# Kernel tuning notes

Hardware: AMD Instinct MI355X
Metric: run time of the kernel (lower is better)

Reference implementation:

```python
import jax, jax.numpy as jnp
import numpy as np

B, M, D, V = 2048, 64, 256, 50000  # batch, max neighbors, embed dim, num_symbols (pad idx = V)
EPS = 1e-5


def _ln(x, g, b):
    mu = jnp.mean(x, axis=-1, keepdims=True)
    var = jnp.var(x, axis=-1, keepdims=True)
    return (x - mu) * jax.lax.rsqrt(var + EPS) * g + b


def _attn(q, k, v, Wq, Wk, Wv, Wb, Wo, bo):
    # q: (B, D); k, v: (B, M, D). num_heads=1, att_size=D. NOTE: self.scale is defined
    # but never used in the original forward, so no scaling here (faithful).
    qh = q @ Wq.T                                   # (B, D)
    kh = jnp.einsum('bmd,ed->bme', k, Wk)           # (B, M, D)
    vh = jnp.einsum('bmd,ed->bme', v, Wv)           # (B, M, D)
    s = jnp.einsum('bd,bmd->bm', qh @ Wb.T, kh)     # bilinear-modulated scores
    a = jax.nn.softmax(s, axis=-1)
    o = jnp.einsum('bm,bmd->bd', a, vh)
    return o @ Wo.T + bo


def setup_inputs() -> dict:
    key = jax.random.key(0)
    ks = jax.random.split(key, 40)
    f = lambda i, shape, s=0.05: (jax.random.normal(ks[i], shape, dtype=jnp.float32) * s)
    emb = f(0, (V + 1, D), 0.1).at[V].set(0.0)  # padding_idx row is zero
    inp = {
        'entity_pairs': jax.random.randint(ks[1], (B, 2), 0, V),
        'left_conn': jax.random.randint(ks[2], (B, M, 2), 0, V),
        'left_deg': jax.random.randint(ks[3], (B,), 0, M),
        'right_conn': jax.random.randint(ks[4], (B, M, 2), 0, V),
        'right_deg': jax.random.randint(ks[5], (B,), 0, M),
        'emb': emb,
        # task-aware attention params
        'Wq_t': f(6, (D, D)), 'Wk_t': f(7, (D, D)), 'Wv_t': f(8, (D, D)),
        'Wbil_t': f(9, (D, D)), 'Wo_t': f(10, (D, D)), 'bo_t': jnp.zeros((D,), jnp.float32),
        # entity-pair attention params
        'Wq_e': f(11, (D, D)), 'Wk_e': f(12, (D, D)), 'Wv_e': f(13, (D, D)),
        'Wbil_e': f(14, (D, D)), 'Wo_e': f(15, (D, D)), 'bo_e': jnp.zeros((D,), jnp.float32),
        'ln_g': jnp.ones((D,), jnp.float32), 'ln_b': jnp.zeros((D,), jnp.float32),
        'Wtail': f(16, (D, D)), 'Whead': f(17, (D, D)),
        'Wrel': f(18, (2 * D, D, D), 0.02),  # nn.Bilinear weight (out, in1, in2), no bias
        'W1': f(19, (2 * D, 2 * D)), 'b1': jnp.zeros((2 * D,), jnp.float32),
        'W2': f(20, (2 * D, 2 * D)),
        'ln1_g': jnp.ones((2 * D,), jnp.float32), 'ln1_b': jnp.zeros((2 * D,), jnp.float32),
        'Wg': f(21, (D, D), 0.3), 'Ug': f(22, (D, D), 0.3), 'bg': jnp.zeros((D,), jnp.float32),
        'Wr': f(23, (D, D), 0.3), 'Ur': f(24, (D, D), 0.3), 'br': jnp.zeros((D,), jnp.float32),
    }
    return inp


def reference(entity_pairs, left_conn, left_deg, right_conn, right_deg, emb,
              Wq_t, Wk_t, Wv_t, Wbil_t, Wo_t, bo_t,
              Wq_e, Wk_e, Wv_e, Wbil_e, Wo_e, bo_e,
              ln_g, ln_b, Wtail, Whead, Wrel, W1, b1, W2, ln1_g, ln1_b,
              Wg, Ug, bg, Wr, Ur, br):
    # eval mode: dropouts are identity
    ent = emb[entity_pairs]                 # (B, 2, D)
    eL, eR = ent[:, 0], ent[:, 1]           # (B, D) each
    rel_L = emb[left_conn[:, :, 0]]         # (B, M, D)
    ent_L = emb[left_conn[:, :, 1]]
    rel_R = emb[right_conn[:, :, 0]]
    ent_R = emb[right_conn[:, :, 1]]

    # rel_w bilinear: (B, 2D) -> split into forward/backward task relation embeddings
    rel_emb = jnp.einsum('bi,oij,bj->bo', eL, Wrel, eR)
    rel_fwd, rel_bwd = rel_emb[:, :D], rel_emb[:, D:]

    # GRU-style neighbor gating
    g = jax.nn.sigmoid(rel_L @ Wg + ent_L @ Ug + bg)
    V_head = jax.nn.relu(g * rel_L + (1.0 - g) * ent_L)
    gr = jax.nn.sigmoid(rel_R @ Wr + ent_R @ Ur + br)
    V_tail = jax.nn.relu(gr * rel_R + (1.0 - gr) * ent_R)

    def enhance(att_out, e):
        h = jax.nn.relu(att_out @ Wtail.T + e @ Whead.T)
        return _ln(h + e, ln_g, ln_b)

    h_rel = _attn(rel_fwd, rel_L, V_head, Wq_t, Wk_t, Wv_t, Wbil_t, Wo_t, bo_t)
    enh_head_ = enhance(h_rel, eL)
    t_rel = _attn(rel_bwd, rel_R, V_tail, Wq_t, Wk_t, Wv_t, Wbil_t, Wo_t, bo_t)
    enh_tail_ = enhance(t_rel, eR)

    h_ent = _attn(enh_tail_, ent_L, V_head, Wq_e, Wk_e, Wv_e, Wbil_e, Wo_e, bo_e)
    enh_head = enhance(h_ent, eL)
    t_ent = _attn(enh_head_, ent_R, V_tail, Wq_e, Wk_e, Wv_e, Wbil_e, Wo_e, bo_e)
    enh_tail = enhance(t_ent, eR)

    pair = jnp.concatenate([enh_head, enh_tail], axis=-1)  # (B, 2D)
    # bi_MLP with residual + LayerNorm
    h = jax.nn.relu(pair @ W1.T + b1)
    h = h @ W2.T
    return _ln(h + pair, ln1_g, ln1_b)
```

## Files before the change

### kernel.cpp

```cpp
#include <hip/hip_runtime.h>
#include <hip/hip_bf16.h>

#define BN 2048
#define MN 64
#define DN 256
#define EMB_ROWS 50001
#define EMB_PAD 50016
#define LN_EPS 1e-5f
#define SPLITK 16

typedef __hip_bfloat16 bf16;
typedef __attribute__((ext_vector_type(8))) short bf16x8;
typedef __attribute__((ext_vector_type(4))) float f32x4;

static __device__ __forceinline__ short f2bf(float f) {
  return __builtin_bit_cast(short, __float2bfloat16(f));
}
static __device__ __forceinline__ float bfu(unsigned short u) {
  unsigned int x = ((unsigned int)u) << 16;
  return __builtin_bit_cast(float, x);
}

typedef __attribute__((address_space(1))) const void g_void;
typedef __attribute__((address_space(3))) void l_void;
static __device__ __forceinline__ void gl_lds16(const void* g, void* l) {
  __builtin_amdgcn_global_load_lds((g_void*)g, (l_void*)l, 16, 0, 0);
}

static __device__ __forceinline__ void dev_mm(float* __restrict__ C, const float* __restrict__ A,
                                              const float* __restrict__ B, int N, int K,
                                              int aI, int aM, int bM, int bJ, int blk, int tid) {
  int idx = blk * 256 + tid;
  int i = idx / N, j = idx - i * N;
  float s = 0.f;
  for (int m = 0; m < K; ++m) s += A[i * aI + m * aM] * B[m * bM + j * bJ];
  C[idx] = s;
}
static __device__ __forceinline__ void dev_tr(float* __restrict__ dst, const float* __restrict__ src,
                                              int rows, int cols, int blk, int tid) {
  int idx = blk * 256 + tid;
  int r = idx / cols, c = idx - r * cols;
  dst[c * rows + r] = src[idx];
}

#define S1_GRID 27349
__global__ void k_stage1(const float* __restrict__ Wbil_t, const float* __restrict__ Wq_t,
                         const float* __restrict__ Wbil_e, const float* __restrict__ Wq_e,
                         const float* __restrict__ Wo_t, const float* __restrict__ Wv_t,
                         const float* __restrict__ Wo_e, const float* __restrict__ Wv_e,
                         const float* __restrict__ Wtail, const float* __restrict__ Whead,
                         const float* __restrict__ W1, const float* __restrict__ W2,
                         const float* __restrict__ Wg, const float* __restrict__ Ug,
                         const float* __restrict__ Wr, const float* __restrict__ Ur,
                         const float* __restrict__ Wrel, const float* __restrict__ emb,
                         const int* __restrict__ pairs,
                         float* __restrict__ T_t, float* __restrict__ T_e,
                         float* __restrict__ Wov_t, float* __restrict__ Wov_e,
                         float* __restrict__ WtailT, float* __restrict__ Whead_kn,
                         float* __restrict__ W1_kn, float* __restrict__ W2_kn,
                         bf16* __restrict__ wcat, bf16* __restrict__ emb_bf,
                         float* __restrict__ eL, float* __restrict__ eR,
                         bf16* __restrict__ eRbf, float* __restrict__ eLT,
                         bf16* __restrict__ Wrel_bf) {
  int bid = blockIdx.x, tid = threadIdx.x;
  if (bid < 256)        dev_mm(T_t, Wbil_t, Wq_t, 256, 256, 256, 1, 256, 1, bid, tid);
  else if (bid < 512)   dev_mm(T_e, Wbil_e, Wq_e, 256, 256, 256, 1, 256, 1, bid - 256, tid);
  else if (bid < 768)   dev_mm(Wov_t, Wo_t, Wv_t, 256, 256, 256, 1, 256, 1, bid - 512, tid);
  else if (bid < 1024)  dev_mm(Wov_e, Wo_e, Wv_e, 256, 256, 256, 1, 256, 1, bid - 768, tid);
  else if (bid < 1280)  dev_tr(WtailT, Wtail, 256, 256, bid - 1024, tid);
  else if (bid < 1536)  dev_tr(Whead_kn, Whead, 256, 256, bid - 1280, tid);
  else if (bid < 2560)  dev_tr(W1_kn, W1, 512, 512, bid - 1536, tid);
  else if (bid < 3584)  dev_tr(W2_kn, W2, 512, 512, bid - 2560, tid);
  else if (bid < 4608) {
    int idx = (bid - 3584) * 256 + tid;
    int n = idx >> 8, k = idx & 255;
    const float* s = (n < 256) ? Wg : (n < 512) ? Ug : (n < 768) ? Wr : Ur;
    wcat[idx] = __float2bfloat16(s[k * 256 + (n & 255)]);
  } else if (bid < 17109) {
    int i = (bid - 4608) * 256 + tid;
    if (i < (EMB_ROWS * 256) / 4) {
      float4 v = ((const float4*)emb)[i];
      ushort4 o;
      o.x = (unsigned short)f2bf(v.x); o.y = (unsigned short)f2bf(v.y);
      o.z = (unsigned short)f2bf(v.z); o.w = (unsigned short)f2bf(v.w);
      ((ushort4*)emb_bf)[i] = o;
    }
  } else if (bid < 19157) {
    int b = bid - 17109, d = tid;
    float vL = emb[(size_t)pairs[2 * b] * 256 + d];
    float vR = emb[(size_t)pairs[2 * b + 1] * 256 + d];
    eL[b * 256 + d] = vL;
    eR[b * 256 + d] = vR;
    eRbf[b * 256 + d] = __float2bfloat16(vR);
    eLT[(size_t)d * BN + b] = vL;
  } else {
    int blk = bid - 19157;
    int base = blk * 1024 + tid;
    #pragma unroll
    for (int it = 0; it < 4; ++it) {
      int i = base + it * 256;
      float4 v = ((const float4*)Wrel)[i];
      ushort4 o;
      o.x = (unsigned short)f2bf(v.x); o.y = (unsigned short)f2bf(v.y);
      o.z = (unsigned short)f2bf(v.z); o.w = (unsigned short)f2bf(v.w);
      ((ushort4*)Wrel_bf)[i] = o;
    }
  }
}

__global__ void k_stage2(const float* __restrict__ T_t, const float* __restrict__ Wk_t, float* __restrict__ Cq_t,
                         const float* __restrict__ T_e, const float* __restrict__ Wk_e, float* __restrict__ Cq_e,
                         const float* __restrict__ Wov_t, const float* __restrict__ WtailT, float* __restrict__ Wenh_t,
                         const float* __restrict__ Wov_e, float* __restrict__ Wenh_e,
                         const float* __restrict__ Wtail, const float* __restrict__ bo_t, const float* __restrict__ bo_e,
                         float* __restrict__ benh_t, float* __restrict__ benh_e) {
  int bid = blockIdx.x, tid = threadIdx.x;
  if (bid < 256)       dev_mm(Cq_t, T_t, Wk_t, 256, 256, 1, 256, 256, 1, bid, tid);
  else if (bid < 512)  dev_mm(Cq_e, T_e, Wk_e, 256, 256, 1, 256, 256, 1, bid - 256, tid);
  else if (bid < 768)  dev_mm(Wenh_t, Wov_t, WtailT, 256, 256, 1, 256, 256, 1, bid - 512, tid);
  else if (bid < 1024) dev_mm(Wenh_e, Wov_e, WtailT, 256, 256, 1, 256, 256, 1, bid - 768, tid);
  else {
    float s1 = 0.f, s2 = 0.f;
    for (int m = 0; m < 256; ++m) {
      float w = Wtail[tid * 256 + m];
      s1 += w * bo_t[m];
      s2 += w * bo_e[m];
    }
    benh_t[tid] = s1;
    benh_e[tid] = s2;
  }
}

__global__ __launch_bounds__(256, 2) void k_e4_gemm(const bf16* __restrict__ embbf,
                                                    const bf16* __restrict__ wcat,
                                                    bf16* __restrict__ E4) {
  int bid = blockIdx.x;
  int lid = (bid & 7) * 392 + (bid >> 3);
  int mchunk = lid >> 4, nt = lid & 15;
  int tid = threadIdx.x;
  int w = tid >> 6, lane = tid & 63;
  int l16 = lane & 15, lq = lane >> 4, kfo = lq * 8;
  int n0 = nt * 64;

  bf16x8 B[4][8];
  #pragma unroll
  for (int nf = 0; nf < 4; ++nf) {
    const bf16* bp = wcat + (size_t)(n0 + nf * 16 + l16) * 256 + kfo;
    #pragma unroll
    for (int ks = 0; ks < 8; ++ks) B[nf][ks] = *(const bf16x8*)(bp + ks * 32);
  }

  f32x4 z = {0.f, 0.f, 0.f, 0.f};
  #pragma unroll
  for (int g = 0; g < 4; ++g) {
    int rbase = mchunk * 256 + w * 64 + g * 16;
    int arow = rbase + l16; if (arow >= EMB_ROWS) arow = EMB_ROWS - 1;
    const bf16* ap = embbf + (size_t)arow * 256 + kfo;
    bf16x8 A[8];
    #pragma unroll
    for (int ks = 0; ks < 8; ++ks) A[ks] = *(const bf16x8*)(ap + ks * 32);
    f32x4 acc[4];
    #pragma unroll
    for (int nf = 0; nf < 4; ++nf) acc[nf] = z;
    #pragma unroll
    for (int ks = 0; ks < 8; ++ks) {
      acc[0] = __builtin_amdgcn_mfma_f32_16x16x32_bf16(A[ks], B[0][ks], acc[0], 0, 0, 0);
      acc[1] = __builtin_amdgcn_mfma_f32_16x16x32_bf16(A[ks], B[1][ks], acc[1], 0, 0, 0);
      acc[2] = __builtin_amdgcn_mfma_f32_16x16x32_bf16(A[ks], B[2][ks], acc[2], 0, 0, 0);
      acc[3] = __builtin_amdgcn_mfma_f32_16x16x32_bf16(A[ks], B[3][ks], acc[3], 0, 0, 0);
    }
    #pragma unroll
    for (int nf = 0; nf < 4; ++nf) {
      int col = n0 + nf * 16 + l16;
      #pragma unroll
      for (int r = 0; r < 4; ++r) {
        int row = rbase + lq * 4 + r;
        if (row < EMB_ROWS) E4[(size_t)row * 1024 + col] = __float2bfloat16(acc[nf][r]);
      }
    }
  }
}

__global__ __launch_bounds__(256, 2) void k_bilinear(const bf16* __restrict__ eRbf,
                                                     const float* __restrict__ eLT,
                                                     const bf16* __restrict__ wrel,
                                                     float* __restrict__ part) {
  __shared__ char bsh[2][8192];
  int bid = blockIdx.x;
  int lid = (bid & 7) * 256 + (bid >> 3);
  int bx = lid & 15, by = (lid >> 4) & 7, bz = lid >> 7;
  int tid = threadIdx.x, w = tid >> 6, lane = tid & 63;
  int l16 = lane & 15, lq = lane >> 4;
  int kfo = lq * 8;
  int m_base = bx * 128 + w * 32;
  int n0 = by * 64;
  int i0 = bz * 16;

  bf16x8 ar[2][8];
  #pragma unroll
  for (int mi = 0; mi < 2; ++mi) {
    const bf16* er = eRbf + (size_t)(m_base + mi * 16 + l16) * 256 + kfo;
    #pragma unroll
    for (int jb = 0; jb < 8; ++jb) ar[mi][jb] = *(const bf16x8*)(er + jb * 32);
  }

  f32x4 z = {0.f, 0.f, 0.f, 0.f};
  f32x4 accF[2][4];
  f32x4 P[2][4];
  #pragma unroll
  for (int mi = 0; mi < 2; ++mi)
    #pragma unroll
    for (int nf = 0; nf < 4; ++nf) { accF[mi][nf] = z; P[mi][nf] = z; }

  int srow = tid >> 3, sblk = tid & 7;
  const bf16* wbase = wrel + (size_t)n0 * 65536 + (size_t)i0 * 256;
  auto stage = [&](int c, int step) {
    size_t so = (size_t)step * 64;
    #pragma unroll
    for (int q = 0; q < 2; ++q) {
      int r = q * 32 + srow;
      const bf16* src = wbase + (size_t)r * 65536 + so + (size_t)((sblk ^ (r & 7)) << 3);
      gl_lds16(src, &bsh[c][q * 4096 + w * 1024]);
    }
  };

  stage(0, 0);
  __syncthreads();
  int cur = 0;
  for (int s = 0; s < 16; ++s) {
    const float* elb = eLT + (size_t)(i0 + s) * BN + m_base + lq * 4;
    float4 el0 = *(const float4*)(elb);
    float4 el1 = *(const float4*)(elb + 16);
    #pragma unroll
    for (int jb4 = 0; jb4 < 4; ++jb4) {
      int step = s * 4 + jb4;
      if (step + 1 < 64) stage(cur ^ 1, step + 1);
      bf16x8 bq[2][4];
      #pragma unroll
      for (int kk = 0; kk < 2; ++kk)
        #pragma unroll
        for (int nf = 0; nf < 4; ++nf) {
          int rl = nf * 16 + l16;
          int blk = (kk * 4 + lq) ^ (l16 & 7);
          bq[kk][nf] = *(const bf16x8*)&bsh[cur][rl * 128 + (blk << 4)];
        }
      #pragma unroll
      for (int kk = 0; kk < 2; ++kk)
        #pragma unroll
        for (int mi = 0; mi < 2; ++mi)
          #pragma unroll
          for (int nf = 0; nf < 4; ++nf) {
            if (jb4 == 0 && kk == 0)
              P[mi][nf] = __builtin_amdgcn_mfma_f32_16x16x32_bf16(ar[mi][jb4 * 2 + kk], bq[kk][nf], z, 0, 0, 0);
            else
              P[mi][nf] = __builtin_amdgcn_mfma_f32_16x16x32_bf16(ar[mi][jb4 * 2 + kk], bq[kk][nf], P[mi][nf], 0, 0, 0);
          }
      __syncthreads();
      cur ^= 1;
    }
    #pragma unroll
    for (int mi = 0; mi < 2; ++mi) {
      float4 el = mi ? el1 : el0;
      #pragma unroll
      for (int nf = 0; nf < 4; ++nf) {
        accF[mi][nf][0] += el.x * P[mi][nf][0];
        accF[mi][nf][1] += el.y * P[mi][nf][1];
        accF[mi][nf][2] += el.z * P[mi][nf][2];
        accF[mi][nf][3] += el.w * P[mi][nf][3];
      }
    }
  }

  float* p = part + (size_t)bz * BN * 512;
  #pragma unroll
  for (int mi = 0; mi < 2; ++mi) {
    #pragma unroll
    for (int nf = 0; nf < 4; ++nf) {
      int col = n0 + nf * 16 + l16;
      #pragma unroll
      for (int r = 0; r < 4; ++r) {
        int row = m_base + mi * 16 + lq * 4 + r;
        p[(size_t)row * 512 + col] = accF[mi][nf][r];
      }
    }
  }
}

__global__ __launch_bounds__(256) void k_vbuild(const int* __restrict__ lconn, const int* __restrict__ rconn,
                                                const bf16* __restrict__ embbf, const bf16* __restrict__ E4,
                                                const float* __restrict__ bg, const float* __restrict__ br,
                                                bf16* __restrict__ Vh, bf16* __restrict__ Vt) {
  int task = blockIdx.x * 4 + (threadIdx.x >> 6);
  int lane = threadIdx.x & 63;
  int d0 = lane * 4;
  {
    int i0 = lconn[2 * task], i1 = lconn[2 * task + 1];
    ushort4 ga = *(const ushort4*)(E4 + (size_t)i0 * 1024 + d0);
    ushort4 gb = *(const ushort4*)(E4 + (size_t)i1 * 1024 + 256 + d0);
    float4 bgv = *(const float4*)(bg + d0);
    ushort4 ea = *(const ushort4*)(embbf + (size_t)i0 * 256 + d0);
    ushort4 eb = *(const ushort4*)(embbf + (size_t)i1 * 256 + d0);
    ushort4 oh;
    {
      float g = 1.f / (1.f + expf(-(bfu(ga.x) + bfu(gb.x) + bgv.x)));
      oh.x = (unsigned short)f2bf(fmaxf(g * bfu(ea.x) + (1.f - g) * bfu(eb.x), 0.f));
      g = 1.f / (1.f + expf(-(bfu(ga.y) + bfu(gb.y) + bgv.y)));
      oh.y = (unsigned short)f2bf(fmaxf(g * bfu(ea.y) + (1.f - g) * bfu(eb.y), 0.f));
      g = 1.f / (1.f + expf(-(bfu(ga.z) + bfu(gb.z) + bgv.z)));
      oh.z = (unsigned short)f2bf(fmaxf(g * bfu(ea.z) + (1.f - g) * bfu(eb.z), 0.f));
      g = 1.f / (1.f + expf(-(bfu(ga.w) + bfu(gb.w) + bgv.w)));
      oh.w = (unsigned short)f2bf(fmaxf(g * bfu(ea.w) + (1.f - g) * bfu(eb.w), 0.f));
    }
    *(ushort4*)(Vh + (size_t)task * 256 + d0) = oh;
  }
  {
    int r0 = rconn[2 * task], r1 = rconn[2 * task + 1];
    ushort4 ga = *(const ushort4*)(E4 + (size_t)r0 * 1024 + 512 + d0);
    ushort4 gb = *(const ushort4*)(E4 + (size_t)r1 * 1024 + 768 + d0);
    float4 brv = *(const float4*)(br + d0);
    ushort4 ea = *(const ushort4*)(embbf + (size_t)r0 * 256 + d0);
    ushort4 eb = *(const ushort4*)(embbf + (size_t)r1 * 256 + d0);
    ushort4 ot;
    {
      float g = 1.f / (1.f + expf(-(bfu(ga.x) + bfu(gb.x) + brv.x)));
      ot.x = (unsigned short)f2bf(fmaxf(g * bfu(ea.x) + (1.f - g) * bfu(eb.x), 0.f));
      g = 1.f / (1.f + expf(-(bfu(ga.y) + bfu(gb.y) + brv.y)));
      ot.y = (unsigned short)f2bf(fmaxf(g * bfu(ea.y) + (1.f - g) * bfu(eb.y), 0.f));
      g = 1.f / (1.f + expf(-(bfu(ga.z) + bfu(gb.z) + brv.z)));
      ot.z = (unsigned short)f2bf(fmaxf(g * bfu(ea.z) + (1.f - g) * bfu(eb.z), 0.f));
      g = 1.f / (1.f + expf(-(bfu(ga.w) + bfu(gb.w) + brv.w)));
      ot.w = (unsigned short)f2bf(fmaxf(g * bfu(ea.w) + (1.f - g) * bfu(eb.w), 0.f));
    }
    *(ushort4*)(Vt + (size_t)task * 256 + d0) = ot;
  }
}

__global__ __launch_bounds__(256) void k_qk12(const float* __restrict__ part, const float* __restrict__ Cq,
                                              float* __restrict__ qkb) {
  __shared__ float xs[16][256];
  int bid = blockIdx.x, tid = threadIdx.x;
  int half = bid >> 7;
  int r0 = (bid & 127) * 16;
  int col0 = half * 256;
  for (int t = tid; t < 16 * 256; t += 256) {
    int r = t >> 8, k = t & 255;
    const float* pp = part + (size_t)(r0 + r) * 512 + col0 + k;
    float s = 0.f;
    #pragma unroll
    for (int z = 0; z < SPLITK; ++z) s += pp[(size_t)z * BN * 512];
    xs[r][k] = s;
  }
  __syncthreads();
  float acc[16];
  #pragma unroll
  for (int r = 0; r < 16; ++r) acc[r] = 0.f;
  for (int k4 = 0; k4 < 256; k4 += 4) {
    float w0 = Cq[(k4 + 0) * 256 + tid];
    float w1 = Cq[(k4 + 1) * 256 + tid];
    float w2 = Cq[(k4 + 2) * 256 + tid];
    float w3 = Cq[(k4 + 3) * 256 + tid];
    #pragma unroll
    for (int r = 0; r < 16; ++r) {
      float4 a = *(const float4*)&xs[r][k4];
      acc[r] += a.x * w0 + a.y * w1 + a.z * w2 + a.w * w3;
    }
  }
  int ob = half * 2048 + r0;
  #pragma unroll
  for (int r = 0; r < 16; ++r) qkb[(size_t)(ob + r) * 256 + tid] = acc[r];
}

__global__ __launch_bounds__(256) void k_qk34(const float* __restrict__ X0, const float* __restrict__ X1,
                                              const float* __restrict__ Cq, float* __restrict__ qkb) {
  __shared__ float xs[16][256];
  int bid = blockIdx.x, tid = threadIdx.x;
  int half = bid >> 7;
  const float* X = half ? X1 : X0;
  int r0 = (bid & 127) * 16;
  for (int t = tid; t < 16 * 256; t += 256) {
    int r = t >> 8, k = t & 255;
    xs[r][k] = X[(size_t)(r0 + r) * 256 + k];
  }
  __syncthreads();
  float acc[16];
  #pragma unroll
  for (int r = 0; r < 16; ++r) acc[r] = 0.f;
  for (int k4 = 0; k4 < 256; k4 += 4) {
    float w0 = Cq[(k4 + 0) * 256 + tid];
    float w1 = Cq[(k4 + 1) * 256 + tid];
    float w2 = Cq[(k4 + 2) * 256 + tid];
    float w3 = Cq[(k4 + 3) * 256 + tid];
    #pragma unroll
    for (int r = 0; r < 16; ++r) {
      float4 a = *(const float4*)&xs[r][k4];
      acc[r] += a.x * w0 + a.y * w1 + a.z * w2 + a.w * w3;
    }
  }
  int ob = half * 2048 + r0;
  #pragma unroll
  for (int r = 0; r < 16; ++r) qkb[(size_t)(ob + r) * 256 + tid] = acc[r];
}

__global__ __launch_bounds__(256) void k_attn_dual(const float* __restrict__ qk,
                                                   const int* __restrict__ lconn, const int* __restrict__ rconn,
                                                   const bf16* __restrict__ Vh, const bf16* __restrict__ Vt,
                                                   int sel, const bf16* __restrict__ embbf,
                                                   float* __restrict__ ov) {
  __shared__ float ss[64];
  __shared__ float as[64];
  __shared__ float ps[4][256];
  int bid = blockIdx.x;
  int b = bid & 2047;
  const int* conn = (bid < 2048) ? lconn : rconn;
  const bf16* Vbuf = (bid < 2048) ? Vh : Vt;
  int tid = threadIdx.x;
  int w = tid >> 6, lane = tid & 63;
  float4 qv = *(const float4*)(qk + (size_t)bid * 256 + lane * 4);
  for (int mi = 0; mi < 16; ++mi) {
    int m = w * 16 + mi;
    int idx = conn[((size_t)b * 64 + m) * 2 + sel];
    ushort4 kr = *(const ushort4*)(embbf + (size_t)idx * 256 + lane * 4);
    float p = qv.x * bfu(kr.x) + qv.y * bfu(kr.y) + qv.z * bfu(kr.z) + qv.w * bfu(kr.w);
    #pragma unroll
    for (int off = 32; off; off >>= 1) p += __shfl_xor(p, off, 64);
    if (lane == 0) ss[m] = p;
  }
  __syncthreads();
  if (w == 0) {
    float v = ss[lane];
    float mx = v;
    #pragma unroll
    for (int off = 32; off; off >>= 1) mx = fmaxf(mx, __shfl_xor(mx, off, 64));
    float e = expf(v - mx);
    float sum = e;
    #pragma unroll
    for (int off = 32; off; off >>= 1) sum += __shfl_xor(sum, off, 64);
    as[lane] = e / sum;
  }
  __syncthreads();
  const bf16* vrow = Vbuf + (size_t)b * 64 * 256;
  float4 a4 = {0.f, 0.f, 0.f, 0.f};
  for (int mi = 0; mi < 16; ++mi) {
    int m = w * 16 + mi;
    float sc = as[m];
    ushort4 v4 = *(const ushort4*)(vrow + (size_t)m * 256 + lane * 4);
    a4.x += sc * bfu(v4.x);
    a4.y += sc * bfu(v4.y);
    a4.z += sc * bfu(v4.z);
    a4.w += sc * bfu(v4.w);
  }
  *(float4*)&ps[w][lane * 4] = a4;
  __syncthreads();
  float o = ps[0][tid] + ps[1][tid] + ps[2][tid] + ps[3][tid];
  ov[(size_t)bid * 256 + tid] = o;
}

__global__ __launch_bounds__(256) void k_enh_dual(const float* __restrict__ ovb,
                                                  const float* __restrict__ e0, const float* __restrict__ e1,
                                                  const float* __restrict__ Wenh_kn, const float* __restrict__ Whead_kn,
                                                  const float* __restrict__ benh, const float* __restrict__ lng,
                                                  const float* __restrict__ lnb,
                                                  float* __restrict__ out0, float* __restrict__ out1,
                                                  int ostride, int ob0, int ob1) {
  __shared__ float x1[16][256];
  __shared__ float x2[16][256];
  __shared__ float stats[16][2];
  int bid = blockIdx.x, tid = threadIdx.x;
  int half = bid >> 7;
  const float* e = half ? e1 : e0;
  float* outp = half ? out1 : out0;
  int obase = half ? ob1 : ob0;
  int r0 = (bid & 127) * 16;
  int ovr0 = half * 2048 + r0;
  for (int t = tid; t < 16 * 256; t += 256) {
    int r = t >> 8, k = t & 255;
    x1[r][k] = ovb[(size_t)(ovr0 + r) * 256 + k];
    x2[r][k] = e[(size_t)(r0 + r) * 256 + k];
  }
  __syncthreads();
  float acc[16];
  #pragma unroll
  for (int r = 0; r < 16; ++r) acc[r] = 0.f;
  for (int k4 = 0; k4 < 256; k4 += 4) {
    float w10 = Wenh_kn[(k4 + 0) * 256 + tid], w11 = Wenh_kn[(k4 + 1) * 256 + tid];
    float w12 = Wenh_kn[(k4 + 2) * 256 + tid], w13 = Wenh_kn[(k4 + 3) * 256 + tid];
    float w20 = Whead_kn[(k4 + 0) * 256 + tid], w21 = Whead_kn[(k4 + 1) * 256 + tid];
    float w22 = Whead_kn[(k4 + 2) * 256 + tid], w23 = Whead_kn[(k4 + 3) * 256 + tid];
    #pragma unroll
    for (int r = 0; r < 16; ++r) {
      float4 a = *(const float4*)&x1[r][k4];
      float4 bb = *(const float4*)&x2[r][k4];
      acc[r] += a.x * w10 + a.y * w11 + a.z * w12 + a.w * w13
              + bb.x * w20 + bb.y * w21 + bb.z * w22 + bb.w * w23;
    }
  }
  float bz = benh[tid];
  float hv[16];
  #pragma unroll
  for (int r = 0; r < 16; ++r) hv[r] = fmaxf(acc[r] + bz, 0.f) + x2[r][tid];
  __syncthreads();
  #pragma unroll
  for (int r = 0; r < 16; ++r) x1[r][tid] = hv[r];
  __syncthreads();
  int w = tid >> 6, lane = tid & 63;
  for (int rr = 0; rr < 4; ++rr) {
    int r = w * 4 + rr;
    float s1 = 0.f, s2 = 0.f;
    #pragma unroll
    for (int jj = 0; jj < 4; ++jj) {
      float v = x1[r][lane + jj * 64];
      s1 += v; s2 += v * v;
    }
    #pragma unroll
    for (int off = 32; off; off >>= 1) {
      s1 += __shfl_xor(s1, off, 64);
      s2 += __shfl_xor(s2, off, 64);
    }
    if (lane == 0) {
      float mu = s1 * (1.f / 256.f);
      float var = s2 * (1.f / 256.f) - mu * mu;
      stats[r][0] = mu;
      stats[r][1] = rsqrtf(var + LN_EPS);
    }
  }
  __syncthreads();
  float gv = lng[tid], bv = lnb[tid];
  #pragma unroll
  for (int r = 0; r < 16; ++r) {
    float v = (x1[r][tid] - stats[r][0]) * stats[r][1] * gv + bv;
    outp[(size_t)(r0 + r) * ostride + obase + tid] = v;
  }
}

__global__ __launch_bounds__(256) void k_lin(const float* __restrict__ X, const float* __restrict__ Wkn,
                                             const float* __restrict__ bias, float* __restrict__ Y,
                                             int Kdim, int Ndim, int act) {
  __shared__ float xs[16][512];
  int tid = threadIdx.x;
  int r0 = blockIdx.x * 16;
  int col = blockIdx.y * 256 + tid;
  for (int t = tid; t < 16 * Kdim; t += 256) {
    int r = t / Kdim, k = t - r * Kdim;
    xs[r][k] = X[(size_t)(r0 + r) * Kdim + k];
  }
  __syncthreads();
  float acc[16];
  #pragma unroll
  for (int r = 0; r < 16; ++r) acc[r] = 0.f;
  for (int k4 = 0; k4 < Kdim; k4 += 4) {
    float w0 = Wkn[(size_t)(k4 + 0) * Ndim + col];
    float w1 = Wkn[(size_t)(k4 + 1) * Ndim + col];
    float w2 = Wkn[(size_t)(k4 + 2) * Ndim + col];
    float w3 = Wkn[(size_t)(k4 + 3) * Ndim + col];
    #pragma unroll
    for (int r = 0; r < 16; ++r) {
      float4 a = *(const float4*)&xs[r][k4];
      acc[r] += a.x * w0 + a.y * w1 + a.z * w2 + a.w * w3;
    }
  }
  float bv = bias ? bias[col] : 0.f;
  #pragma unroll
  for (int r = 0; r < 16; ++r) {
    float v = acc[r] + bv;
    if (act) v = fmaxf(v, 0.f);
    Y[(size_t)(r0 + r) * Ndim + col] = v;
  }
}

__global__ __launch_bounds__(256) void k_mlp2ln(const float* __restrict__ h1, const float* __restrict__ W2kn,
                                                const float* __restrict__ pairb, const float* __restrict__ g,
                                                const float* __restrict__ bb, float* __restrict__ out) {
  __shared__ float xs[16][512];
  __shared__ float stats[16][2];
  int bid = blockIdx.x, tid = threadIdx.x;
  int r0 = bid * 16;
  for (int t = tid; t < 16 * 512; t += 256) {
    int r = t >> 9, k = t & 511;
    xs[r][k] = h1[(size_t)(r0 + r) * 512 + k];
  }
  __syncthreads();
  float acc0[16], acc1[16];
  #pragma unroll
  for (int r = 0; r < 16; ++r) { acc0[r] = 0.f; acc1[r] = 0.f; }
  for (int k4 = 0; k4 < 512; k4 += 4) {
    float a0 = W2kn[(size_t)(k4 + 0) * 512 + tid];
    float a1 = W2kn[(size_t)(k4 + 1) * 512 + tid];
    float a2 = W2kn[(size_t)(k4 + 2) * 512 + tid];
    float a3 = W2kn[(size_t)(k4 + 3) * 512 + tid];
    float b0 = W2kn[(size_t)(k4 + 0) * 512 + tid + 256];
    float b1 = W2kn[(size_t)(k4 + 1) * 512 + tid + 256];
    float b2 = W2kn[(size_t)(k4 + 2) * 512 + tid + 256];
    float b3 = W2kn[(size_t)(k4 + 3) * 512 + tid + 256];
    #pragma unroll
    for (int r = 0; r < 16; ++r) {
      float4 a = *(const float4*)&xs[r][k4];
      acc0[r] += a.x * a0 + a.y * a1 + a.z * a2 + a.w * a3;
      acc1[r] += a.x * b0 + a.y * b1 + a.z * b2 + a.w * b3;
    }
  }
  __syncthreads();
  #pragma unroll
  for (int r = 0; r < 16; ++r) {
    xs[r][tid]       = acc0[r] + pairb[(size_t)(r0 + r) * 512 + tid];
    xs[r][tid + 256] = acc1[r] + pairb[(size_t)(r0 + r) * 512 + tid + 256];
  }
  __syncthreads();
  int w = tid >> 6, lane = tid & 63;
  for (int rr = 0; rr < 4; ++rr) {
    int r = w * 4 + rr;
    float s1 = 0.f, s2 = 0.f;
    #pragma unroll
    for (int jj = 0; jj < 8; ++jj) {
      float v = xs[r][lane + jj * 64];
      s1 += v; s2 += v * v;
    }
    #pragma unroll
    for (int off = 32; off; off >>= 1) {
      s1 += __shfl_xor(s1, off, 64);
      s2 += __shfl_xor(s2, off, 64);
    }
    if (lane == 0) {
      float mu = s1 * (1.f / 512.f);
      stats[r][0] = mu;
      stats[r][1] = rsqrtf(s2 * (1.f / 512.f) - mu * mu + LN_EPS);
    }
  }
  __syncthreads();
  float g0 = g[tid], g1 = g[tid + 256], b0v = bb[tid], b1v = bb[tid + 256];
  #pragma unroll
  for (int r = 0; r < 16; ++r) {
    float mu = stats[r][0], rstd = stats[r][1];
    out[(size_t)(r0 + r) * 512 + tid]       = (xs[r][tid] - mu) * rstd * g0 + b0v;
    out[(size_t)(r0 + r) * 512 + tid + 256] = (xs[r][tid + 256] - mu) * rstd * g1 + b1v;
  }
}

extern "C" void kernel_launch(void* const* d_in, const int* in_sizes, int n_in,
                              void* d_out, int out_size, void* d_ws, size_t ws_size,
                              hipStream_t stream) {
  (void)in_sizes; (void)n_in; (void)out_size; (void)ws_size;
  const int*   entity_pairs = (const int*)d_in[0];
  const int*   left_conn    = (const int*)d_in[1];
  const int*   right_conn   = (const int*)d_in[3];
  const float* emb    = (const float*)d_in[5];
  const float* Wq_t   = (const float*)d_in[6];
  const float* Wk_t   = (const float*)d_in[7];
  const float* Wv_t   = (const float*)d_in[8];
  const float* Wbil_t = (const float*)d_in[9];
  const float* Wo_t   = (const float*)d_in[10];
  const float* bo_t   = (const float*)d_in[11];
  const float* Wq_e   = (const float*)d_in[12];
  const float* Wk_e   = (const float*)d_in[13];
  const float* Wv_e   = (const float*)d_in[14];
  const float* Wbil_e = (const float*)d_in[15];
  const float* Wo_e   = (const float*)d_in[16];
  const float* bo_e   = (const float*)d_in[17];
  const float* ln_g   = (const float*)d_in[18];
  const float* ln_b   = (const float*)d_in[19];
  const float* Wtail  = (const float*)d_in[20];
  const float* Whead  = (const float*)d_in[21];
  const float* Wrel   = (const float*)d_in[22];
  const float* W1     = (const float*)d_in[23];
  const float* b1     = (const float*)d_in[24];
  const float* W2     = (const float*)d_in[25];
  const float* ln1_g  = (const float*)d_in[26];
  const float* ln1_b  = (const float*)d_in[27];
  const float* Wg     = (const float*)d_in[28];
  const float* Ug     = (const float*)d_in[29];
  const float* bg     = (const float*)d_in[30];
  const float* Wr     = (const float*)d_in[31];
  const float* Ur     = (const float*)d_in[32];
  const float* br     = (const float*)d_in[33];
  float* out = (float*)d_out;

  char* wp = (char*)d_ws;
  auto alloc = [&](size_t bytes) -> void* {
    void* p = (void*)wp;
    wp += (bytes + 255) & ~(size_t)255;
    return p;
  };
  bf16* Wrel_bf = (bf16*)alloc((size_t)512 * 65536 * 2);
  bf16* emb_bf  = (bf16*)alloc((size_t)EMB_PAD * 256 * 2);
  bf16* E4      = (bf16*)alloc((size_t)EMB_PAD * 1024 * 2);
  bf16* wcat    = (bf16*)alloc((size_t)1024 * 256 * 2);
  bf16* Vh      = (bf16*)alloc((size_t)BN * MN * 256 * 2);
  bf16* Vt      = (bf16*)alloc((size_t)BN * MN * 256 * 2);
  bf16* eRbf_g  = (bf16*)alloc((size_t)BN * 256 * 2);
  float* eLT    = (float*)alloc((size_t)256 * BN * 4);
  float* eLp     = (float*)alloc((size_t)BN * 256 * 4);
  float* eRp     = (float*)alloc((size_t)BN * 256 * 4);
  float* bil_part= (float*)alloc((size_t)SPLITK * BN * 512 * 4);
  float* qkbuf   = (float*)alloc((size_t)2 * BN * 256 * 4);
  float* ovbuf   = (float*)alloc((size_t)2 * BN * 256 * 4);
  float* enh_h   = (float*)alloc((size_t)BN * 256 * 4);
  float* enh_t   = (float*)alloc((size_t)BN * 256 * 4);
  float* pairb   = (float*)alloc((size_t)BN * 512 * 4);
  float* h1buf   = (float*)alloc((size_t)BN * 512 * 4);
  float* T_t     = (float*)alloc(256 * 256 * 4);
  float* Cq_t    = (float*)alloc(256 * 256 * 4);
  float* Wov_t   = (float*)alloc(256 * 256 * 4);
  float* Wenh_t  = (float*)alloc(256 * 256 * 4);
  float* benh_t  = (float*)alloc(256 * 4);
  float* T_e     = (float*)alloc(256 * 256 * 4);
  float* Cq_e    = (float*)alloc(256 * 256 * 4);
  float* Wov_e   = (float*)alloc(256 * 256 * 4);
  float* Wenh_e  = (float*)alloc(256 * 256 * 4);
  float* benh_e  = (float*)alloc(256 * 4);
  float* Whead_kn= (float*)alloc(256 * 256 * 4);
  float* WtailT  = (float*)alloc(256 * 256 * 4);
  float* W1_kn   = (float*)alloc(512 * 512 * 4);
  float* W2_kn   = (float*)alloc(512 * 512 * 4);

  k_stage1<<<S1_GRID, 256, 0, stream>>>(Wbil_t, Wq_t, Wbil_e, Wq_e, Wo_t, Wv_t, Wo_e, Wv_e,
                                        Wtail, Whead, W1, W2, Wg, Ug, Wr, Ur, Wrel, emb,
                                        entity_pairs,
                                        T_t, T_e, Wov_t, Wov_e, WtailT, Whead_kn, W1_kn, W2_kn,
                                        wcat, emb_bf, eLp, eRp, eRbf_g, eLT, Wrel_bf);
  k_stage2<<<1025, 256, 0, stream>>>(T_t, Wk_t, Cq_t, T_e, Wk_e, Cq_e,
                                     Wov_t, WtailT, Wenh_t, Wov_e, Wenh_e,
                                     Wtail, bo_t, bo_e, benh_t, benh_e);
  k_e4_gemm<<<3136, 256, 0, stream>>>(emb_bf, wcat, E4);
  k_bilinear<<<2048, 256, 0, stream>>>(eRbf_g, eLT, Wrel_bf, bil_part);
  k_vbuild<<<(BN * MN) / 4, 256, 0, stream>>>(left_conn, right_conn, emb_bf, E4, bg, br, Vh, Vt);

  k_qk12<<<256, 256, 0, stream>>>(bil_part, Cq_t, qkbuf);
  k_attn_dual<<<4096, 256, 0, stream>>>(qkbuf, left_conn, right_conn, Vh, Vt, 0, emb_bf, ovbuf);
  k_enh_dual<<<256, 256, 0, stream>>>(ovbuf, eLp, eRp, Wenh_t, Whead_kn, benh_t, ln_g, ln_b,
                                      enh_h, enh_t, 256, 0, 0);
  k_qk34<<<256, 256, 0, stream>>>(enh_t, enh_h, Cq_e, qkbuf);
  k_attn_dual<<<4096, 256, 0, stream>>>(qkbuf, left_conn, right_conn, Vh, Vt, 1, emb_bf, ovbuf);
  k_enh_dual<<<256, 256, 0, stream>>>(ovbuf, eLp, eRp, Wenh_e, Whead_kn, benh_e, ln_g, ln_b,
                                      pairb, pairb, 512, 0, 256);

  k_lin<<<dim3(128, 2), 256, 0, stream>>>(pairb, W1_kn, b1, h1buf, 512, 512, 1);
  k_mlp2ln<<<128, 256, 0, stream>>>(h1buf, W2_kn, pairb, ln1_g, ln1_b, out);
}
```

Before: 980.6 us.

## Merge stage2, E4 GEMM and bilinear into one launch with deeper LDS pipeline

Combines the weight-precompute kernel, the embedding projection GEMM and the bilinear relation kernel into a single heterogeneous launch, so that independent work can run at the same time and fewer launch boundaries are paid. The vbuild and qk12 kernels are also merged into one launch. The bilinear kernel now processes 32 input rows per block, halving split-K from 16 to 8 and shrinking the partial-sum buffer. It uses a 4-deep global-to-LDS ring buffer with explicit vmcnt waits and raw barriers instead of double buffering. The cost is more LDS per block (32KB), which may limit occupancy for the co-scheduled E4 and dev_mm blocks, and fewer bilinear blocks for parallelism.

```diff
diff --git a/kernel.cpp b/kernel.cpp
--- a/kernel.cpp
+++ b/kernel.cpp
@@ -7,7 +7,9 @@
 #define EMB_ROWS 50001
 #define EMB_PAD 50016
 #define LN_EPS 1e-5f
-#define SPLITK 16
+#define SPLITK 8
+#define KCHUNK 8192
+#define TSTEPS 128
 
 typedef __hip_bfloat16 bf16;
 typedef __attribute__((ext_vector_type(8))) short bf16x8;
@@ -108,33 +110,120 @@
   }
 }
 
-__global__ void k_stage2(const float* __restrict__ T_t, const float* __restrict__ Wk_t, float* __restrict__ Cq_t,
-                         const float* __restrict__ T_e, const float* __restrict__ Wk_e, float* __restrict__ Cq_e,
-                         const float* __restrict__ Wov_t, const float* __restrict__ WtailT, float* __restrict__ Wenh_t,
-                         const float* __restrict__ Wov_e, float* __restrict__ Wenh_e,
-                         const float* __restrict__ Wtail, const float* __restrict__ bo_t, const float* __restrict__ bo_e,
-                         float* __restrict__ benh_t, float* __restrict__ benh_e) {
-  int bid = blockIdx.x, tid = threadIdx.x;
-  if (bid < 256)       dev_mm(Cq_t, T_t, Wk_t, 256, 256, 1, 256, 256, 1, bid, tid);
-  else if (bid < 512)  dev_mm(Cq_e, T_e, Wk_e, 256, 256, 1, 256, 256, 1, bid - 256, tid);
-  else if (bid < 768)  dev_mm(Wenh_t, Wov_t, WtailT, 256, 256, 1, 256, 256, 1, bid - 512, tid);
-  else if (bid < 1024) dev_mm(Wenh_e, Wov_e, WtailT, 256, 256, 1, 256, 256, 1, bid - 768, tid);
-  else {
-    float s1 = 0.f, s2 = 0.f;
-    for (int m = 0; m < 256; ++m) {
-      float w = Wtail[tid * 256 + m];
-      s1 += w * bo_t[m];
-      s2 += w * bo_e[m];
-    }
-    benh_t[tid] = s1;
-    benh_e[tid] = s2;
-  }
-}
-
-__global__ __launch_bounds__(256, 2) void k_e4_gemm(const bf16* __restrict__ embbf,
-                                                    const bf16* __restrict__ wcat,
-                                                    bf16* __restrict__ E4) {
-  int bid = blockIdx.x;
+static __device__ __forceinline__ void dev_bilinear(char (*bsh)[8192], int bid,
+                                                    const bf16* __restrict__ eRbf,
+                                                    const float* __restrict__ eLT,
+                                                    const bf16* __restrict__ wrel,
+                                                    float* __restrict__ part) {
+  int lid = (bid & 7) * 128 + (bid >> 3);
+  int bx = lid & 15, by = (lid >> 4) & 7, bz = lid >> 7;
+  int tid = threadIdx.x, w = tid >> 6, lane = tid & 63;
+  int l16 = lane & 15, lq = lane >> 4;
+  int kfo = lq * 8;
+  int m_base = bx * 128 + w * 32;
+  int n0 = by * 64;
+  int i0 = bz * 32;
+
+  bf16x8 ar[2][8];
+  #pragma unroll
+  for (int mi = 0; mi < 2; ++mi) {
+    const bf16* er = eRbf + (size_t)(m_base + mi * 16 + l16) * 256 + kfo;
+    #pragma unroll
+    for (int jb = 0; jb < 8; ++jb) ar[mi][jb] = *(const bf16x8*)(er + jb * 32);
+  }
+
+  f32x4 z = {0.f, 0.f, 0.f, 0.f};
+  f32x4 accF[2][4];
+  f32x4 P[2][4];
+  #pragma unroll
+  for (int mi = 0; mi < 2; ++mi)
+    #pragma unroll
+    for (int nf = 0; nf < 4; ++nf) { accF[mi][nf] = z; P[mi][nf] = z; }
+
+  int srow = tid >> 3, sblk = tid & 7;
+  const bf16* wbase = wrel + (size_t)n0 * 65536 + (size_t)i0 * 256;
+  auto stage = [&](int c, int step) {
+    size_t so = (size_t)step * 64;
+    #pragma unroll
+    for (int q = 0; q < 2; ++q) {
+      int r = q * 32 + srow;
+      const bf16* src = wbase + (size_t)r * 65536 + so + (size_t)((sblk ^ (r & 7)) << 3);
+      gl_lds16(src, &bsh[c][q * 4096 + w * 1024]);
+    }
+  };
+
+  stage(0, 0); stage(1, 1); stage(2, 2);
+  float4 el0 = {0,0,0,0}, el1 = {0,0,0,0};
+  for (int t = 0; t < TSTEPS; ++t) {
+    if ((t & 3) == 0) {
+      int s = t >> 2;
+      const float* elb = eLT + (size_t)(i0 + s) * BN + m_base + lq * 4;
+      el0 = *(const float4*)(elb);
+      el1 = *(const float4*)(elb + 16);
+      #pragma unroll
+      for (int mi = 0; mi < 2; ++mi)
+        #pragma unroll
+        for (int nf = 0; nf < 4; ++nf) P[mi][nf] = z;
+    }
+    if (t + 3 < TSTEPS) stage((t + 3) & 3, t + 3);
+    __builtin_amdgcn_sched_barrier(0);
+    if (t + 3 < TSTEPS) { asm volatile("s_waitcnt vmcnt(6)" ::: "memory"); }
+    else                { asm volatile("s_waitcnt vmcnt(0)" ::: "memory"); }
+    __builtin_amdgcn_s_barrier();
+    __builtin_amdgcn_sched_barrier(0);
+    const char* bufp = bsh[t & 3];
+    #pragma unroll
+    for (int kk = 0; kk < 2; ++kk) {
+      bf16x8 bq[4];
+      #pragma unroll
+      for (int nf = 0; nf < 4; ++nf) {
+        int rl = nf * 16 + l16;
+        int blk = (kk * 4 + lq) ^ (l16 & 7);
+        bq[nf] = *(const bf16x8*)&bufp[rl * 128 + (blk << 4)];
+      }
+      int jb = (t & 3) * 2 + kk;
+      #pragma unroll
+      for (int mi = 0; mi < 2; ++mi)
+        #pragma unroll
+        for (int nf = 0; nf < 4; ++nf)
+          P[mi][nf] = __builtin_amdgcn_mfma_f32_16x16x32_bf16(ar[mi][jb], bq[nf], P[mi][nf], 0, 0, 0);
+    }
+    if ((t & 3) == 3) {
+      #pragma unroll
+      for (int mi = 0; mi < 2; ++mi) {
+        float4 el = mi ? el1 : el0;
+        #pragma unroll
+        for (int nf = 0; nf < 4; ++nf) {
+          accF[mi][nf][0] += el.x * P[mi][nf][0];
+          accF[mi][nf][1] += el.y * P[mi][nf][1];
+          accF[mi][nf][2] += el.z * P[mi][nf][2];
+          accF[mi][nf][3] += el.w * P[mi][nf][3];
+        }
+      }
+    }
+    __builtin_amdgcn_sched_barrier(0);
+    asm volatile("s_waitcnt lgkmcnt(0)" ::: "memory");
+    __builtin_amdgcn_s_barrier();
+    __builtin_amdgcn_sched_barrier(0);
+  }
+
+  float* p = part + (size_t)bz * BN * 512;
+  #pragma unroll
+  for (int mi = 0; mi < 2; ++mi) {
+    #pragma unroll
+    for (int nf = 0; nf < 4; ++nf) {
+      int col = n0 + nf * 16 + l16;
+      #pragma unroll
+      for (int r = 0; r < 4; ++r) {
+        int row = m_base + mi * 16 + lq * 4 + r;
+        p[(size_t)row * 512 + col] = accF[mi][nf][r];
+      }
+    }
+  }
+}
+
+static __device__ __forceinline__ void dev_e4(int bid, const bf16* __restrict__ embbf,
+                                              const bf16* __restrict__ wcat, bf16* __restrict__ E4) {
   int lid = (bid & 7) * 392 + (bid >> 3);
   int mchunk = lid >> 4, nt = lid & 15;
   int tid = threadIdx.x;
@@ -181,116 +270,51 @@
   }
 }
 
-__global__ __launch_bounds__(256, 2) void k_bilinear(const bf16* __restrict__ eRbf,
-                                                     const float* __restrict__ eLT,
-                                                     const bf16* __restrict__ wrel,
-                                                     float* __restrict__ part) {
-  __shared__ char bsh[2][8192];
-  int bid = blockIdx.x;
-  int lid = (bid & 7) * 256 + (bid >> 3);
-  int bx = lid & 15, by = (lid >> 4) & 7, bz = lid >> 7;
-  int tid = threadIdx.x, w = tid >> 6, lane = tid & 63;
-  int l16 = lane & 15, lq = lane >> 4;
-  int kfo = lq * 8;
-  int m_base = bx * 128 + w * 32;
-  int n0 = by * 64;
-  int i0 = bz * 16;
-
-  bf16x8 ar[2][8];
-  #pragma unroll
-  for (int mi = 0; mi < 2; ++mi) {
-    const bf16* er = eRbf + (size_t)(m_base + mi * 16 + l16) * 256 + kfo;
-    #pragma unroll
-    for (int jb = 0; jb < 8; ++jb) ar[mi][jb] = *(const bf16x8*)(er + jb * 32);
-  }
-
-  f32x4 z = {0.f, 0.f, 0.f, 0.f};
-  f32x4 accF[2][4];
-  f32x4 P[2][4];
-  #pragma unroll
-  for (int mi = 0; mi < 2; ++mi)
-    #pragma unroll
-    for (int nf = 0; nf < 4; ++nf) { accF[mi][nf] = z; P[mi][nf] = z; }
-
-  int srow = tid >> 3, sblk = tid & 7;
-  const bf16* wbase = wrel + (size_t)n0 * 65536 + (size_t)i0 * 256;
-  auto stage = [&](int c, int step) {
-    size_t so = (size_t)step * 64;
-    #pragma unroll
-    for (int q = 0; q < 2; ++q) {
-      int r = q * 32 + srow;
-      const bf16* src = wbase + (size_t)r * 65536 + so + (size_t)((sblk ^ (r & 7)) << 3);
-      gl_lds16(src, &bsh[c][q * 4096 + w * 1024]);
-    }
-  };
-
-  stage(0, 0);
-  __syncthreads();
-  int cur = 0;
-  for (int s = 0; s < 16; ++s) {
-    const float* elb = eLT + (size_t)(i0 + s) * BN + m_base + lq * 4;
-    float4 el0 = *(const float4*)(elb);
-    float4 el1 = *(const float4*)(elb + 16);
-    #pragma unroll
-    for (int jb4 = 0; jb4 < 4; ++jb4) {
-      int step = s * 4 + jb4;
-      if (step + 1 < 64) stage(cur ^ 1, step + 1);
-      bf16x8 bq[2][4];
-      #pragma unroll
-      for (int kk = 0; kk < 2; ++kk)
-        #pragma unroll
-        for (int nf = 0; nf < 4; ++nf) {
-          int rl = nf * 16 + l16;
-          int blk = (kk * 4 + lq) ^ (l16 & 7);
-          bq[kk][nf] = *(const bf16x8*)&bsh[cur][rl * 128 + (blk << 4)];
-        }
-      #pragma unroll
-      for (int kk = 0; kk < 2; ++kk)
-        #pragma unroll
-        for (int mi = 0; mi < 2; ++mi)
-          #pragma unroll
-          for (int nf = 0; nf < 4; ++nf) {
-            if (jb4 == 0 && kk == 0)
-              P[mi][nf] = __builtin_amdgcn_mfma_f32_16x16x32_bf16(ar[mi][jb4 * 2 + kk], bq[kk][nf], z, 0, 0, 0);
-            else
-              P[mi][nf] = __builtin_amdgcn_mfma_f32_16x16x32_bf16(ar[mi][jb4 * 2 + kk], bq[kk][nf], P[mi][nf], 0, 0, 0);
-          }
-      __syncthreads();
-      cur ^= 1;
-    }
-    #pragma unroll
-    for (int mi = 0; mi < 2; ++mi) {
-      float4 el = mi ? el1 : el0;
-      #pragma unroll
-      for (int nf = 0; nf < 4; ++nf) {
-        accF[mi][nf][0] += el.x * P[mi][nf][0];
-        accF[mi][nf][1] += el.y * P[mi][nf][1];
-        accF[mi][nf][2] += el.z * P[mi][nf][2];
-        accF[mi][nf][3] += el.w * P[mi][nf][3];
+__global__ __launch_bounds__(256, 2) void k_heavy(const bf16* __restrict__ eRbf, const float* __restrict__ eLT,
+                                                  const bf16* __restrict__ wrel, float* __restrict__ part,
+                                                  const bf16* __restrict__ embbf, const bf16* __restrict__ wcat,
+                                                  bf16* __restrict__ E4,
+                                                  const float* __restrict__ T_t, const float* __restrict__ Wk_t,
+                                                  float* __restrict__ Cq_t,
+                                                  const float* __restrict__ T_e, const float* __restrict__ Wk_e,
+                                                  float* __restrict__ Cq_e,
+                                                  const float* __restrict__ Wov_t, const float* __restrict__ WtailT,
+                                                  float* __restrict__ Wenh_t,
+                                                  const float* __restrict__ Wov_e, float* __restrict__ Wenh_e,
+                                                  const float* __restrict__ Wtail, const float* __restrict__ bo_t,
+                                                  const float* __restrict__ bo_e,
+                                                  float* __restrict__ benh_t, float* __restrict__ benh_e) {
+  __shared__ char bsh[4][8192];
+  int bid = blockIdx.x, tid = threadIdx.x;
+  if (bid < 1024) {
+    dev_bilinear(bsh, bid, eRbf, eLT, wrel, part);
+  } else if (bid < 4160) {
+    dev_e4(bid - 1024, embbf, wcat, E4);
+  } else {
+    int b2 = bid - 4160;
+    if (b2 < 256)       dev_mm(Cq_t, T_t, Wk_t, 256, 256, 1, 256, 256, 1, b2, tid);
+    else if (b2 < 512)  dev_mm(Cq_e, T_e, Wk_e, 256, 256, 1, 256, 256, 1, b2 - 256, tid);
+    else if (b2 < 768)  dev_mm(Wenh_t, Wov_t, WtailT, 256, 256, 1, 256, 256, 1, b2 - 512, tid);
+    else if (b2 < 1024) dev_mm(Wenh_e, Wov_e, WtailT, 256, 256, 1, 256, 256, 1, b2 - 768, tid);
+    else {
+      float s1 = 0.f, s2 = 0.f;
+      for (int m = 0; m < 256; ++m) {
+        float wv = Wtail[tid * 256 + m];
+        s1 += wv * bo_t[m];
+        s2 += wv * bo_e[m];
       }
-    }
-  }
-
-  float* p = part + (size_t)bz * BN * 512;
-  #pragma unroll
-  for (int mi = 0; mi < 2; ++mi) {
-    #pragma unroll
-    for (int nf = 0; nf < 4; ++nf) {
-      int col = n0 + nf * 16 + l16;
-      #pragma unroll
-      for (int r = 0; r < 4; ++r) {
-        int row = m_base + mi * 16 + lq * 4 + r;
-        p[(size_t)row * 512 + col] = accF[mi][nf][r];
-      }
-    }
-  }
-}
-
-__global__ __launch_bounds__(256) void k_vbuild(const int* __restrict__ lconn, const int* __restrict__ rconn,
-                                                const bf16* __restrict__ embbf, const bf16* __restrict__ E4,
-                                                const float* __restrict__ bg, const float* __restrict__ br,
-                                                bf16* __restrict__ Vh, bf16* __restrict__ Vt) {
-  int task = blockIdx.x * 4 + (threadIdx.x >> 6);
+      benh_t[tid] = s1;
+      benh_e[tid] = s2;
+    }
+  }
+}
+
+static __device__ __forceinline__ void dev_vbuild(int bid, const int* __restrict__ lconn,
+                                                  const int* __restrict__ rconn,
+                                                  const bf16* __restrict__ embbf, const bf16* __restrict__ E4,
+                                                  const float* __restrict__ bg, const float* __restrict__ br,
+                                                  bf16* __restrict__ Vh, bf16* __restrict__ Vt) {
+  int task = bid * 4 + (threadIdx.x >> 6);
   int lane = threadIdx.x & 63;
   int d0 = lane * 4;
   {
@@ -335,19 +359,28 @@
   }
 }
 
-__global__ __launch_bounds__(256) void k_qk12(const float* __restrict__ part, const float* __restrict__ Cq,
-                                              float* __restrict__ qkb) {
+__global__ __launch_bounds__(256) void k_vq(const int* __restrict__ lconn, const int* __restrict__ rconn,
+                                            const bf16* __restrict__ embbf, const bf16* __restrict__ E4,
+                                            const float* __restrict__ bg, const float* __restrict__ br,
+                                            bf16* __restrict__ Vh, bf16* __restrict__ Vt,
+                                            const float* __restrict__ part, const float* __restrict__ Cq,
+                                            float* __restrict__ qkb) {
   __shared__ float xs[16][256];
   int bid = blockIdx.x, tid = threadIdx.x;
-  int half = bid >> 7;
-  int r0 = (bid & 127) * 16;
+  if (bid < 32768) {
+    dev_vbuild(bid, lconn, rconn, embbf, E4, bg, br, Vh, Vt);
+    return;
+  }
+  int b2 = bid - 32768;
+  int half = b2 >> 7;
+  int r0 = (b2 & 127) * 16;
   int col0 = half * 256;
   for (int t = tid; t < 16 * 256; t += 256) {
     int r = t >> 8, k = t & 255;
     const float* pp = part + (size_t)(r0 + r) * 512 + col0 + k;
     float s = 0.f;
     #pragma unroll
-    for (int z = 0; z < SPLITK; ++z) s += pp[(size_t)z * BN * 512];
+    for (int zc = 0; zc < SPLITK; ++zc) s += pp[(size_t)zc * BN * 512];
     xs[r][k] = s;
   }
   __syncthreads();
@@ -716,14 +749,13 @@
                                         entity_pairs,
                                         T_t, T_e, Wov_t, Wov_e, WtailT, Whead_kn, W1_kn, W2_kn,
                                         wcat, emb_bf, eLp, eRp, eRbf_g, eLT, Wrel_bf);
-  k_stage2<<<1025, 256, 0, stream>>>(T_t, Wk_t, Cq_t, T_e, Wk_e, Cq_e,
-                                     Wov_t, WtailT, Wenh_t, Wov_e, Wenh_e,
-                                     Wtail, bo_t, bo_e, benh_t, benh_e);
-  k_e4_gemm<<<3136, 256, 0, stream>>>(emb_bf, wcat, E4);
-  k_bilinear<<<2048, 256, 0, stream>>>(eRbf_g, eLT, Wrel_bf, bil_part);
-  k_vbuild<<<(BN * MN) / 4, 256, 0, stream>>>(left_conn, right_conn, emb_bf, E4, bg, br, Vh, Vt);
-
-  k_qk12<<<256, 256, 0, stream>>>(bil_part, Cq_t, qkbuf);
+  k_heavy<<<5185, 256, 0, stream>>>(eRbf_g, eLT, Wrel_bf, bil_part,
+                                    emb_bf, wcat, E4,
+                                    T_t, Wk_t, Cq_t, T_e, Wk_e, Cq_e,
+                                    Wov_t, WtailT, Wenh_t, Wov_e, Wenh_e,
+                                    Wtail, bo_t, bo_e, benh_t, benh_e);
+  k_vq<<<33024, 256, 0, stream>>>(left_conn, right_conn, emb_bf, E4, bg, br, Vh, Vt,
+                                  bil_part, Cq_t, qkbuf);
   k_attn_dual<<<4096, 256, 0, stream>>>(qkbuf, left_conn, right_conn, Vh, Vt, 0, emb_bf, ovbuf);
   k_enh_dual<<<256, 256, 0, stream>>>(ovbuf, eLp, eRp, Wenh_t, Whead_kn, benh_t, ln_g, ln_b,
                                       enh_h, enh_t, 256, 0, 0);
```

Result: slower. 1.173 ms (+19.7%).
